# Performance work log

Measured on AMD Instinct MI355X. Metric: run time of the kernel, lower is better.

The kernel has to match this reference:

```python
import jax, jax.numpy as jnp
import numpy as np

B, L, C_IN, H, MID = 8192, 256, 6, 32, 128  # batch, knots, input_channels, hidden_channels, MLP width


def setup_inputs() -> dict:
    key = jax.random.key(0)
    ks = jax.random.split(key, 8)
    cshape = (B, L - 1, C_IN)
    times = jnp.arange(L, dtype=jnp.float32)
    # spline coefficients (a, b, two_c, three_d); small scale keeps the CDE stable
    coeff_a = jax.random.normal(ks[0], cshape, dtype=jnp.float32) * 0.05
    coeff_b = jax.random.normal(ks[1], cshape, dtype=jnp.float32) * 0.05
    coeff_c = jax.random.normal(ks[2], cshape, dtype=jnp.float32) * 0.05
    coeff_d = jax.random.normal(ks[3], cshape, dtype=jnp.float32) * 0.05
    # CDEFunc params: Linear(H->128), Linear(128->H*C_IN); readout Linear(H->C_IN)
    W1 = jax.random.normal(ks[4], (H, MID), dtype=jnp.float32) / np.float32(np.sqrt(H))
    b1 = jnp.zeros((MID,), dtype=jnp.float32)
    W2 = jax.random.normal(ks[5], (MID, H * C_IN), dtype=jnp.float32) / np.float32(np.sqrt(MID))
    b2 = jnp.zeros((H * C_IN,), dtype=jnp.float32)
    Wl = jax.random.normal(ks[6], (H, C_IN), dtype=jnp.float32) / np.float32(np.sqrt(H))
    bl = jnp.zeros((C_IN,), dtype=jnp.float32)
    return dict(times=times, coeff_a=coeff_a, coeff_b=coeff_b, coeff_c=coeff_c,
                coeff_d=coeff_d, W1=W1, b1=b1, W2=W2, b2=b2, Wl=Wl, bl=bl)


def reference(times, coeff_a, coeff_b, coeff_c, coeff_d, W1, b1, W2, b2, Wl, bl):
    # dz/dt = f(z) @ dX/dt, integrated t[0] -> t[-1] (RK4, one step per spline interval).
    def vf(z, dx):
        h = jnp.tanh(z @ W1 + b1)                       # (B, 128)
        g = (h @ W2 + b2).reshape(z.shape[0], H, C_IN)  # (B, H, C_IN)
        return jnp.einsum('bhi,bi->bh', g, dx)          # (B, H)

    dts = times[1:] - times[:-1]                        # (L-1,)
    bs = jnp.moveaxis(coeff_b, 1, 0)                    # (L-1, B, C)
    cs = jnp.moveaxis(coeff_c, 1, 0)
    ds = jnp.moveaxis(coeff_d, 1, 0)
    z0 = jnp.zeros((coeff_b.shape[0], H), dtype=times.dtype)

    def step(z, xs):
        dt, bi, ci, di = xs
        dX = lambda f: bi + ci * f + di * (f * f)       # spline derivative b + 2c*f + 3d*f^2
        k1 = vf(z, dX(0.0))
        k2 = vf(z + 0.5 * dt * k1, dX(0.5 * dt))
        k3 = vf(z + 0.5 * dt * k2, dX(0.5 * dt))
        k4 = vf(z + dt * k3, dX(dt))
        return z + (dt / 6.0) * (k1 + 2.0 * k2 + 2.0 * k3 + k4), None

    zT, _ = jax.lax.scan(step, z0, (dts, bs, cs, ds))
    return zT @ Wl + bl                                 # (B, C_IN)
```

## Files before the change

### kernel.cpp

```cpp
#include <hip/hip_runtime.h>


typedef short short8  __attribute__((ext_vector_type(8)));
typedef short short4v __attribute__((ext_vector_type(4)));
typedef float floatx4 __attribute__((ext_vector_type(4)));

constexpr int B_TOT  = 8192;
constexpr int L      = 256;
constexpr int CIN    = 6;
constexpr int H      = 32;
constexpr int MID    = 128;
constexpr int NSTEPS = L - 1;
constexpr int NB     = 16;
constexpr int WG     = 256;

constexpr int HP  = 152;
constexpr int ZSP = 72;
constexpr int GIS = 33;
constexpr int GBS = 199;
constexpr int ZP  = 33;

__device__ __forceinline__ short f2bf(float x) {
    unsigned u = __builtin_bit_cast(unsigned, x);
    unsigned r = (u + 0x7FFFu + ((u >> 16) & 1u)) >> 16;
    return (short)r;
}
__device__ __forceinline__ float bf2f(short b) {
    unsigned u = ((unsigned)(unsigned short)b) << 16;
    return __builtin_bit_cast(float, u);
}

__global__ __launch_bounds__(WG, 2)
void cde_hybrid_kernel(const float* __restrict__ times,
                       const float* __restrict__ coeff_b,
                       const float* __restrict__ coeff_c,
                       const float* __restrict__ coeff_d,
                       const float* __restrict__ W1g,
                       const float* __restrict__ b1g,
                       const float* __restrict__ W2g,
                       const float* __restrict__ b2g,
                       const float* __restrict__ Wlg,
                       const float* __restrict__ blg,
                       float* __restrict__ out)
{
    __shared__ __align__(16) short sHh[NB][HP], sHm[NB][HP], sHl[NB][HP];
    __shared__ float sGf[NB * GBS + 4];
    __shared__ __align__(16) short sZh[NB][ZSP], sZm[NB][ZSP], sZl[NB][ZSP];
    __shared__ float sZb[NB][ZP], sZa[NB][ZP];
    __shared__ float sDx[3][NB][8];

    const int tid  = threadIdx.x;
    const int lane = tid & 63;
    const int wave = tid >> 6;
    const int l15  = lane & 15;
    const int q    = lane >> 4;
    const int b0   = blockIdx.x * NB;

    short8 w2h[3][4], w2m[3][4], w2l[3][4];
    float  b2v[3];
    int    gofs[3];
    #pragma unroll
    for (int f = 0; f < 3; ++f) {
        const int n = (wave * 3 + f) * 16 + l15;
        b2v[f]  = b2g[n];
        gofs[f] = (n % 6) * GIS + (n / 6);
        #pragma unroll
        for (int ks = 0; ks < 4; ++ks) {
            #pragma unroll
            for (int j = 0; j < 8; ++j) {
                const float w = W2g[(ks * 32 + q * 8 + j) * (H * CIN) + n];
                const short hh = f2bf(w);        const float r1 = w - bf2f(hh);
                const short mm = f2bf(r1);       const float r2 = r1 - bf2f(mm);
                w2h[f][ks][j] = hh; w2m[f][ks][j] = mm; w2l[f][ks][j] = f2bf(r2);
            }
        }
    }

    short8 w1h[2], w1m[2], w1l[2];
    float  b1v[2][4];
    #pragma unroll
    for (int f1 = 0; f1 < 2; ++f1) {
        const int mt = wave * 2 + f1;
        #pragma unroll
        for (int j = 0; j < 8; ++j) {
            const float w = W1g[(q * 8 + j) * MID + mt * 16 + l15];
            const short hh = f2bf(w);        const float r1 = w - bf2f(hh);
            const short mm = f2bf(r1);       const float r2 = r1 - bf2f(mm);
            w1h[f1][j] = hh; w1m[f1][j] = mm; w1l[f1][j] = f2bf(r2);
        }
        #pragma unroll
        for (int r = 0; r < 4; ++r)
            b1v[f1][r] = b1g[mt * 16 + q * 4 + r];
    }

    for (int i = tid; i < NB * ZP; i += WG) {
        (&sZb[0][0])[i] = 0.f; (&sZa[0][0])[i] = 0.f;
    }
    for (int i = tid; i < NB * ZSP; i += WG) {
        (&sZh[0][0])[i] = 0; (&sZm[0][0])[i] = 0; (&sZl[0][0])[i] = 0;
    }
    __syncthreads();

    for (int t = 0; t < NSTEPS; ++t) {
        const float dt = times[t + 1] - times[t];
        if (tid < NB * CIN) {
            const int bb = tid / CIN, ii = tid - bb * CIN;
            const size_t off = ((size_t)(b0 + bb) * NSTEPS + t) * CIN + ii;
            const float vb = coeff_b[off], vc = coeff_c[off], vd = coeff_d[off];
            const float f1 = 0.5f * dt;
            sDx[0][bb][ii] = vb;
            sDx[1][bb][ii] = vb + vc * f1 + vd * f1 * f1;
            sDx[2][bb][ii] = vb + vc * dt + vd * dt * dt;
        }
        __syncthreads();

        #pragma unroll 1
        for (int s = 0; s < 4; ++s) {
            const short8 zh = *(const short8*)&sZh[l15][q * 8];
            const short8 zm = *(const short8*)&sZm[l15][q * 8];
            const short8 zl = *(const short8*)&sZl[l15][q * 8];
            floatx4 ht[2];
            #pragma unroll
            for (int f1 = 0; f1 < 2; ++f1) ht[f1] = floatx4{0.f, 0.f, 0.f, 0.f};
            #pragma unroll
            for (int f1 = 0; f1 < 2; ++f1) {
                ht[f1] = __builtin_amdgcn_mfma_f32_16x16x32_bf16(w1h[f1], zh, ht[f1], 0, 0, 0);
                ht[f1] = __builtin_amdgcn_mfma_f32_16x16x32_bf16(w1h[f1], zm, ht[f1], 0, 0, 0);
                ht[f1] = __builtin_amdgcn_mfma_f32_16x16x32_bf16(w1m[f1], zh, ht[f1], 0, 0, 0);
                ht[f1] = __builtin_amdgcn_mfma_f32_16x16x32_bf16(w1h[f1], zl, ht[f1], 0, 0, 0);
                ht[f1] = __builtin_amdgcn_mfma_f32_16x16x32_bf16(w1m[f1], zm, ht[f1], 0, 0, 0);
                ht[f1] = __builtin_amdgcn_mfma_f32_16x16x32_bf16(w1l[f1], zh, ht[f1], 0, 0, 0);
            }
            #pragma unroll
            for (int f1 = 0; f1 < 2; ++f1) {
                const int mt = wave * 2 + f1;
                short4v vh, vm, vl;
                #pragma unroll
                for (int r = 0; r < 4; ++r) {
                    const float pre = ht[f1][r] + b1v[f1][r];
                    const float e = __expf(2.f * pre);
                    const float h = 1.f - 2.f / (e + 1.f);
                    const short hh = f2bf(h);   const float r1 = h - bf2f(hh);
                    const short hm = f2bf(r1);  const float r2 = r1 - bf2f(hm);
                    vh[r] = hh; vm[r] = hm; vl[r] = f2bf(r2);
                }
                *(short4v*)&sHh[l15][mt * 16 + q * 4] = vh;
                *(short4v*)&sHm[l15][mt * 16 + q * 4] = vm;
                *(short4v*)&sHl[l15][mt * 16 + q * 4] = vl;
            }
            __syncthreads();

            floatx4 g[3];
            #pragma unroll
            for (int f = 0; f < 3; ++f) g[f] = floatx4{0.f, 0.f, 0.f, 0.f};
            #pragma unroll
            for (int ks = 0; ks < 4; ++ks) {
                const short8 ah = *(const short8*)&sHh[l15][ks * 32 + q * 8];
                const short8 am = *(const short8*)&sHm[l15][ks * 32 + q * 8];
                const short8 al = *(const short8*)&sHl[l15][ks * 32 + q * 8];
                #pragma unroll
                for (int f = 0; f < 3; ++f) {
                    g[f] = __builtin_amdgcn_mfma_f32_16x16x32_bf16(ah, w2h[f][ks], g[f], 0, 0, 0);
                    g[f] = __builtin_amdgcn_mfma_f32_16x16x32_bf16(ah, w2m[f][ks], g[f], 0, 0, 0);
                    g[f] = __builtin_amdgcn_mfma_f32_16x16x32_bf16(am, w2h[f][ks], g[f], 0, 0, 0);
                    g[f] = __builtin_amdgcn_mfma_f32_16x16x32_bf16(ah, w2l[f][ks], g[f], 0, 0, 0);
                    g[f] = __builtin_amdgcn_mfma_f32_16x16x32_bf16(am, w2m[f][ks], g[f], 0, 0, 0);
                    g[f] = __builtin_amdgcn_mfma_f32_16x16x32_bf16(al, w2h[f][ks], g[f], 0, 0, 0);
                }
            }
            #pragma unroll
            for (int f = 0; f < 3; ++f) {
                #pragma unroll
                for (int r = 0; r < 4; ++r)
                    sGf[(q * 4 + r) * GBS + gofs[f]] = g[f][r] + b2v[f];
            }
            __syncthreads();

            const int dsel = (s == 0) ? 0 : ((s == 3) ? 2 : 1);
            const float ws = (s == 0 || s == 3) ? dt * (1.f / 6.f) : dt * (1.f / 3.f);
            #pragma unroll
            for (int jj = 0; jj < 2; ++jj) {
                const int pp = tid + 256 * jj;
                const int b = pp >> 5, o = pp & 31;
                float k = 0.f;
                #pragma unroll
                for (int i = 0; i < 6; ++i)
                    k += sGf[b * GBS + i * GIS + o] * sDx[dsel][b][i];
                const float za = sZa[b][o] + ws * k;
                sZa[b][o] = za;
                float zc;
                if (s < 3) {
                    zc = sZb[b][o] + ((s == 2) ? dt : 0.5f * dt) * k;
                } else {
                    sZb[b][o] = za;
                    zc = za;
                }
                const short zh0 = f2bf(zc);  const float zr1 = zc - bf2f(zh0);
                const short zm0 = f2bf(zr1); const float zr2 = zr1 - bf2f(zm0);
                sZh[b][o] = zh0; sZm[b][o] = zm0; sZl[b][o] = f2bf(zr2);
            }
            __syncthreads();
        }
    }

    if (tid < NB * CIN) {
        const int bb = tid / CIN, c = tid - bb * CIN;
        float acc = blg[c];
        #pragma unroll
        for (int o = 0; o < H; ++o) acc += sZb[bb][o] * Wlg[o * CIN + c];
        out[(size_t)(b0 + bb) * CIN + c] = acc;
    }
}

extern "C" void kernel_launch(void* const* d_in, const int* in_sizes, int n_in,
                              void* d_out, int out_size, void* d_ws, size_t ws_size,
                              hipStream_t stream) {
    const float* times = (const float*)d_in[0];
    const float* cb = (const float*)d_in[2];
    const float* cc = (const float*)d_in[3];
    const float* cd = (const float*)d_in[4];
    const float* W1 = (const float*)d_in[5];
    const float* b1 = (const float*)d_in[6];
    const float* W2 = (const float*)d_in[7];
    const float* b2 = (const float*)d_in[8];
    const float* Wl = (const float*)d_in[9];
    const float* bl = (const float*)d_in[10];
    float* out = (float*)d_out;

    hipLaunchKernelGGL(cde_hybrid_kernel, dim3(B_TOT / NB), dim3(WG), 0, stream,
                       times, cb, cc, cd, W1, b1, W2, b2, Wl, bl, out);
}
```

Measured before the change: 2.553 ms.

## Make G-to-k contraction wave-local and keep RK4 state in registers

```diff
diff --git a/kernel.cpp b/kernel.cpp
--- a/kernel.cpp
+++ b/kernel.cpp
@@ -16,8 +16,8 @@
 
 constexpr int HP  = 152;
 constexpr int ZSP = 72;
-constexpr int GIS = 33;
-constexpr int GBS = 199;
+constexpr int GRS = 53;
+constexpr int GWS = 16 * GRS;
 constexpr int ZP  = 33;
 
 __device__ __forceinline__ short f2bf(float x) {
@@ -44,10 +44,10 @@
                        float* __restrict__ out)
 {
     __shared__ __align__(16) short sHh[NB][HP], sHm[NB][HP], sHl[NB][HP];
-    __shared__ float sGf[NB * GBS + 4];
+    __shared__ float sGw[4][GWS];
     __shared__ __align__(16) short sZh[NB][ZSP], sZm[NB][ZSP], sZl[NB][ZSP];
-    __shared__ float sZb[NB][ZP], sZa[NB][ZP];
     __shared__ float sDx[3][NB][8];
+    __shared__ float sFin[NB][ZP];
 
     const int tid  = threadIdx.x;
     const int lane = tid & 63;
@@ -56,14 +56,15 @@
     const int q    = lane >> 4;
     const int b0   = blockIdx.x * NB;
 
+    const int cb = lane & 15;
+    const int co = lane >> 4;
+
     short8 w2h[3][4], w2m[3][4], w2l[3][4];
     float  b2v[3];
-    int    gofs[3];
     #pragma unroll
     for (int f = 0; f < 3; ++f) {
         const int n = (wave * 3 + f) * 16 + l15;
-        b2v[f]  = b2g[n];
-        gofs[f] = (n % 6) * GIS + (n / 6);
+        b2v[f] = b2g[n];
         #pragma unroll
         for (int ks = 0; ks < 4; ++ks) {
             #pragma unroll
@@ -93,9 +94,8 @@
             b1v[f1][r] = b1g[mt * 16 + q * 4 + r];
     }
 
-    for (int i = tid; i < NB * ZP; i += WG) {
-        (&sZb[0][0])[i] = 0.f; (&sZa[0][0])[i] = 0.f;
-    }
+    float za[2] = {0.f, 0.f};
+    float zb[2] = {0.f, 0.f};
     for (int i = tid; i < NB * ZSP; i += WG) {
         (&sZh[0][0])[i] = 0; (&sZm[0][0])[i] = 0; (&sZl[0][0])[i] = 0;
     }
@@ -172,42 +172,46 @@
             for (int f = 0; f < 3; ++f) {
                 #pragma unroll
                 for (int r = 0; r < 4; ++r)
-                    sGf[(q * 4 + r) * GBS + gofs[f]] = g[f][r] + b2v[f];
-            }
-            __syncthreads();
+                    sGw[wave][(q * 4 + r) * GRS + f * 16 + l15] = g[f][r] + b2v[f];
+            }
+            asm volatile("s_waitcnt lgkmcnt(0)" ::: "memory");
+            __builtin_amdgcn_sched_barrier(0);
 
             const int dsel = (s == 0) ? 0 : ((s == 3) ? 2 : 1);
             const float ws = (s == 0 || s == 3) ? dt * (1.f / 6.f) : dt * (1.f / 3.f);
             #pragma unroll
-            for (int jj = 0; jj < 2; ++jj) {
-                const int pp = tid + 256 * jj;
-                const int b = pp >> 5, o = pp & 31;
+            for (int j = 0; j < 2; ++j) {
+                const int ol = co + 4 * j;
                 float k = 0.f;
                 #pragma unroll
                 for (int i = 0; i < 6; ++i)
-                    k += sGf[b * GBS + i * GIS + o] * sDx[dsel][b][i];
-                const float za = sZa[b][o] + ws * k;
-                sZa[b][o] = za;
+                    k += sGw[wave][cb * GRS + 6 * ol + i] * sDx[dsel][cb][i];
+                const float zan = za[j] + ws * k;
+                za[j] = zan;
                 float zc;
                 if (s < 3) {
-                    zc = sZb[b][o] + ((s == 2) ? dt : 0.5f * dt) * k;
+                    zc = zb[j] + ((s == 2) ? dt : 0.5f * dt) * k;
                 } else {
-                    sZb[b][o] = za;
-                    zc = za;
+                    zb[j] = zan;
+                    zc = zan;
                 }
+                const int o = 8 * wave + ol;
                 const short zh0 = f2bf(zc);  const float zr1 = zc - bf2f(zh0);
                 const short zm0 = f2bf(zr1); const float zr2 = zr1 - bf2f(zm0);
-                sZh[b][o] = zh0; sZm[b][o] = zm0; sZl[b][o] = f2bf(zr2);
+                sZh[cb][o] = zh0; sZm[cb][o] = zm0; sZl[cb][o] = f2bf(zr2);
             }
             __syncthreads();
         }
     }
 
+    sFin[cb][8 * wave + co]     = zb[0];
+    sFin[cb][8 * wave + co + 4] = zb[1];
+    __syncthreads();
     if (tid < NB * CIN) {
         const int bb = tid / CIN, c = tid - bb * CIN;
         float acc = blg[c];
         #pragma unroll
-        for (int o = 0; o < H; ++o) acc += sZb[bb][o] * Wlg[o * CIN + c];
+        for (int o = 0; o < H; ++o) acc += sFin[bb][o] * Wlg[o * CIN + c];
         out[(size_t)(b0 + bb) * CIN + c] = acc;
     }
 }
```

After: 2.838 ms. 11.2% more time.
